# Performance work log

Measured on AMD Instinct MI355X. Metric: run time of the kernel, lower is better.

## Reference

```python
import jax, jax.numpy as jnp
import numpy as np

D = 128   # hidden_size
L = 50    # mailbox length (USER_MAX_LEN / ITEM_MAX_LEN)
NU = 8192 # num user nodes
NI = 8192 # num item nodes


def setup_inputs() -> dict:
    key = jax.random.key(0)
    ks = jax.random.split(key, 16)
    s = 0.05
    return {
        "user": jax.random.normal(ks[0], (NU, D), jnp.float32),
        "item": jax.random.normal(ks[1], (NI, D), jnp.float32),
        "W_user": jax.random.normal(ks[2], (D, D), jnp.float32) * s,
        "W_item": jax.random.normal(ks[3], (D, D), jnp.float32) * s,
        "agg_gate_user": jax.random.normal(ks[4], (2 * D, D), jnp.float32) * s,
        "agg_gate_item": jax.random.normal(ks[5], (2 * D, D), jnp.float32) * s,
        "update_user": jax.random.normal(ks[6], (2 * D, D), jnp.float32) * s,
        "update_item": jax.random.normal(ks[7], (2 * D, D), jnp.float32) * s,
        "user_date_emb": jax.random.normal(ks[8], (L, D), jnp.float32) * s,
        "user_date_emb_k": jax.random.normal(ks[9], (L, D), jnp.float32) * s,
        "item_date_emb": jax.random.normal(ks[10], (L, D), jnp.float32) * s,
        "item_date_emb_k": jax.random.normal(ks[11], (L, D), jnp.float32) * s,
        "user_nbr": jax.random.randint(ks[12], (NU, L), 0, NI, jnp.int64) if jax.config.jax_enable_x64 else jax.random.randint(ks[12], (NU, L), 0, NI, jnp.int32),
        "user_nbr_time": jax.random.randint(ks[13], (NU, L), 0, 1000000, jnp.int32),
        "item_nbr": jax.random.randint(ks[14], (NI, L), 0, NU, jnp.int32),
        "item_nbr_time": jax.random.randint(ks[15], (NI, L), 0, 1000000, jnp.int32),
    }


def _reduce(dst_h, src_mail, time, emb, emb_k, gate_W):
    # dst_h: [N,d], src_mail: [N,L,d], time: [N,L]
    # double argsort -> rank; reorder = L - rank - 1 (time-order position)
    order = jnp.argsort(jnp.argsort(time, axis=1), axis=1)
    reorder = time.shape[1] - order - 1                     # [N,L]
    scale = 1.0 / jnp.sqrt(jnp.asarray(dst_h.shape[-1], dst_h.dtype))
    # long-term attention with positional injection
    e = jnp.sum((emb[reorder] + src_mail) * dst_h[:, None, :], axis=-1) * scale
    alpha = jax.nn.softmax(e, axis=1)                       # [N,L]
    h_long = jnp.einsum('nl,nld->nd', alpha, src_mail + emb_k[reorder])
    # short-term attention against most-recent neighbor
    last = jnp.argmax(time, axis=1)                         # [N]
    last_emb = jnp.take_along_axis(src_mail, last[:, None, None], axis=1)  # [N,1,d]
    e1 = jnp.sum(last_emb * src_mail, axis=-1) * scale
    alpha1 = jax.nn.softmax(e1, axis=1)
    h_short = jnp.einsum('nl,nld->nd', alpha1, src_mail)
    return jnp.concatenate([h_long, h_short], axis=-1) @ gate_W  # [N,d]


def reference(user, item, W_user, W_item, agg_gate_user, agg_gate_item,
              update_user, update_item, user_date_emb, user_date_emb_k,
              item_date_emb, item_date_emb_k, user_nbr, user_nbr_time,
              item_nbr, item_nbr_time):
    # feat_drop/attn_drop are identity (eval mode)
    uh = user @ W_user   # [NU,d]
    ih = item @ W_item   # [NI,d]
    # user nodes aggregate item-neighbor mailboxes
    user_agg = _reduce(uh, ih[user_nbr], user_nbr_time,
                       user_date_emb, user_date_emb_k, agg_gate_user)
    # item nodes aggregate user-neighbor mailboxes
    item_agg = _reduce(ih, uh[item_nbr], item_nbr_time,
                       item_date_emb, item_date_emb_k, agg_gate_item)
    user_out = jnp.tanh(jnp.concatenate([user_agg, user], axis=-1) @ update_user)
    item_out = jnp.tanh(jnp.concatenate([item_agg, item], axis=-1) @ update_item)
    return user_out, item_out
```

## Files before the change

### kernel.cpp

```cpp
#include <hip/hip_runtime.h>
#include <math.h>

#define D 128
#define L 50
#define SCALE 0.08838834764831845f

using bf16x8 = __attribute__((ext_vector_type(8))) short;
using f32x4  = __attribute__((ext_vector_type(4))) float;

__device__ __forceinline__ unsigned f2bf(float x) {
    union { float f; unsigned u; } v; v.f = x;
    return (v.u + 0x7fffu + ((v.u >> 16) & 1u)) >> 16;
}
__device__ __forceinline__ float bflo(unsigned u) {
    union { unsigned u; float f; } v; v.u = u << 16; return v.f;
}
__device__ __forceinline__ float bfhi(unsigned u) {
    union { unsigned u; float f; } v; v.u = u & 0xffff0000u; return v.f;
}

__global__ __launch_bounds__(256) void prep1_kernel(
    const float* __restrict__ Wu, const float* __restrict__ Wi,
    const float* __restrict__ ue, const float* __restrict__ ie,
    const float* __restrict__ gu, const float* __restrict__ gi,
    const float* __restrict__ uu, const float* __restrict__ ui,
    float* __restrict__ GUu, float* __restrict__ GUi,
    unsigned short* __restrict__ Bptu, unsigned short* __restrict__ Bpti,
    unsigned short* __restrict__ Btu, unsigned short* __restrict__ Bti)
{
    int b = blockIdx.x, t = threadIdx.x;
    if (b < 50) {
        int side = b / 25;
        int o = (b % 25) * 256 + t;
        int d = o / L, l = o % L;
        const float* W = side ? Wi : Wu;
        const float* E = side ? ie : ue;
        unsigned short* Bpt = side ? Bpti : Bptu;
        float a = 0.f;
        for (int k = 0; k < D; ++k) a += W[d * D + k] * E[l * D + k];
        Bpt[(128 + l) * 128 + d] = (unsigned short)f2bf(a);
    } else if (b < 306) {
        int bb = b - 50;
        int side = bb / 128;
        int o = (bb % 128) * 256 + t;
        int r = o >> 7, c = o & 127;
        const float* G = side ? gi : gu;
        const float* U = side ? ui : uu;
        float* GU      = side ? GUi : GUu;
        unsigned short* Bt = side ? Bti : Btu;
        float a = 0.f;
        for (int k = 0; k < D; ++k) a += G[r * D + k] * U[k * D + c];
        GU[r * D + c] = a;
        Bt[c * 448 + r] = (unsigned short)f2bf(a);
    } else if (b < 434) {
        int bb = b - 306;
        int side = bb >> 6;
        int o = (bb & 63) * 256 + t;
        int r = o >> 7, c = o & 127;
        const float* U = side ? ui : uu;
        unsigned short* Bt = side ? Bti : Btu;
        Bt[c * 448 + 320 + r] = (unsigned short)f2bf(U[(128 + r) * D + c]);
        if (r < 14) Bt[c * 448 + 306 + r] = 0;
    } else if (b < 562) {
        int bb = b - 434;
        int side = bb >> 6;
        int o = (bb & 63) * 256 + t;
        int k = o >> 7, c = o & 127;
        const float* W = side ? Wi : Wu;
        unsigned short* Bpt = side ? Bpti : Bptu;
        Bpt[c * 128 + k] = (unsigned short)f2bf(W[k * D + c]);
    } else {
        int side = b - 562;
        unsigned short* Bpt = side ? Bpti : Bptu;
        for (int j = 0; j < 7; ++j)
            Bpt[178 * 128 + t * 7 + j] = 0;
    }
}

__global__ __launch_bounds__(256) void prep2_kernel(
    const float* __restrict__ uek, const float* __restrict__ iek,
    const float* __restrict__ GUu, const float* __restrict__ GUi,
    unsigned short* __restrict__ Btu, unsigned short* __restrict__ Bti)
{
    int b = blockIdx.x, t = threadIdx.x;
    int side = b / 25;
    int o = (b % 25) * 256 + t;
    int r = o >> 7, c = o & 127;
    const float* EK = side ? iek : uek;
    const float* GU = side ? GUi : GUu;
    unsigned short* Bt = side ? Bti : Btu;
    float a = 0.f;
    for (int k = 0; k < D; ++k) a += EK[r * D + k] * GU[k * D + c];
    Bt[c * 448 + 256 + r] = (unsigned short)f2bf(a);
}

__global__ __launch_bounds__(256) void proj_mfma(
    const float* __restrict__ Xu, const float* __restrict__ Xi,
    const unsigned* __restrict__ Bptu32, const unsigned* __restrict__ Bpti32,
    unsigned* __restrict__ h32, float* __restrict__ eproj,
    unsigned* __restrict__ A32, int NU)
{
    __shared__ __align__(16) unsigned As[32 * 20];
    __shared__ __align__(16) unsigned Bs[192 * 20];
    int t = threadIdx.x;
    int nb = blockIdx.x * 32;
    const float* X = (nb < NU) ? Xu : Xi;
    int xoff = (nb < NU) ? 0 : NU;
    const unsigned* Bt = (nb < NU) ? Bptu32 : Bpti32;
    int wave = t >> 6, lane = t & 63;
    int m16 = lane & 15, quad = lane >> 4;

    f32x4 acc[2][3];
    for (int i = 0; i < 2; ++i)
        for (int j = 0; j < 3; ++j) acc[i][j] = (f32x4){0.f, 0.f, 0.f, 0.f};

    for (int kc = 0; kc < 4; ++kc) {
        if (t < 128) {
            int row = t >> 2, q = t & 3;
            int n = nb + row;
            const float* src = &X[(size_t)(n - xoff) * D + kc * 32 + q * 8];
            float4 v0 = *(const float4*)&src[0];
            float4 v1 = *(const float4*)&src[4];
            uint4 pk;
            pk.x = f2bf(v0.x) | (f2bf(v0.y) << 16);
            pk.y = f2bf(v0.z) | (f2bf(v0.w) << 16);
            pk.z = f2bf(v1.x) | (f2bf(v1.y) << 16);
            pk.w = f2bf(v1.z) | (f2bf(v1.w) << 16);
            *(uint4*)&As[row * 20 + q * 4] = pk;
            *(uint4*)&A32[(size_t)n * 224 + 160 + kc * 16 + q * 4] = pk;
        }
        #pragma unroll
        for (int i = 0; i < 3; ++i) {
            int idx = t * 3 + i;
            int c = idx >> 2, q = idx & 3;
            uint4 v = *(const uint4*)&Bt[(size_t)c * 64 + kc * 16 + q * 4];
            *(uint4*)&Bs[c * 20 + q * 4] = v;
        }
        __syncthreads();
        bf16x8 a0 = *(const bf16x8*)&As[m16 * 20 + quad * 4];
        bf16x8 a1 = *(const bf16x8*)&As[(16 + m16) * 20 + quad * 4];
        #pragma unroll
        for (int ni = 0; ni < 3; ++ni) {
            bf16x8 bb = *(const bf16x8*)&Bs[(wave * 48 + ni * 16 + m16) * 20 + quad * 4];
            acc[0][ni] = __builtin_amdgcn_mfma_f32_16x16x32_bf16(a0, bb, acc[0][ni], 0, 0, 0);
            acc[1][ni] = __builtin_amdgcn_mfma_f32_16x16x32_bf16(a1, bb, acc[1][ni], 0, 0, 0);
        }
        __syncthreads();
    }
    #pragma unroll
    for (int mi = 0; mi < 2; ++mi)
        #pragma unroll
        for (int ni = 0; ni < 3; ++ni) {
            int col = wave * 48 + ni * 16 + m16;
            #pragma unroll
            for (int r = 0; r < 4; ++r) {
                float me = acc[mi][ni][r];
                float pr = __shfl_xor(me, 1);
                int row = nb + mi * 16 + quad * 4 + r;
                if (col < 128) {
                    if (!(lane & 1))
                        h32[(size_t)row * 64 + (col >> 1)] = f2bf(me) | (f2bf(pr) << 16);
                } else if (col < 178) {
                    eproj[(size_t)row * L + (col - 128)] = me;
                }
            }
        }
}

__global__ __launch_bounds__(256) void agg_kernel(
    const unsigned* __restrict__ h32, const float* __restrict__ eproj,
    const int* __restrict__ unbr, const int* __restrict__ untime,
    const int* __restrict__ inbr, const int* __restrict__ intime,
    unsigned* __restrict__ A32, int NU, int NI)
{
    __shared__ unsigned smail[2][L * 64];
    __shared__ unsigned shb[2][64];
    __shared__ float salpha[2][L], salpha1[2][L];
    __shared__ int stime[2][L], sreorder[2][L], snbr[2][L], slast[2];

    int tb = threadIdx.x;
    int sub = tb >> 7;
    int t = tb & 127;
    int g = blockIdx.x * 2 + sub;
    int wave = t >> 6, lane = t & 63;

    const unsigned* mail; const int* nbrp; const int* timp;
    if (g < NU) { mail = h32 + (size_t)NU * 64; nbrp = unbr + (size_t)g * L;        timp = untime + (size_t)g * L; }
    else        { mail = h32;                   nbrp = inbr + (size_t)(g - NU) * L; timp = intime + (size_t)(g - NU) * L; }

    if (t < 64) shb[sub][t] = h32[(size_t)g * 64 + t];
    if (t < L) { stime[sub][t] = timp[t]; snbr[sub][t] = nbrp[t]; }
    __syncthreads();

    if (t < L) {
        int ti = stime[sub][t]; int rank = 0; bool firstmax = true;
        for (int j = 0; j < L; ++j) {
            int tj = stime[sub][j];
            rank += (tj < ti) || (tj == ti && j < t);
            firstmax = firstmax && ((tj < ti) || (tj == ti && j >= t));
        }
        sreorder[sub][t] = L - 1 - rank;
        if (firstmax) slast[sub] = t;
    }
    {
        int q = t >> 5, p = t & 31;
        #pragma unroll
        for (int i = 0; i < 13; ++i) {
            int l = i * 4 + q;
            if (l < L) {
                uint2 v = *(const uint2*)&mail[(size_t)snbr[sub][l] * 64 + p * 2];
                *(uint2*)&smail[sub][l * 64 + 2 * (p ^ (l & 31))] = v;
            }
        }
    }
    __syncthreads();

    float sc = -1e30f;
    if (lane < L) {
        int xr = lane & 31;
        const unsigned* mrow = &smail[sub][lane * 64];
        if (wave == 0) {
            float a = 0.f;
            for (int p = 0; p < 32; ++p) {
                uint2 mv = *(const uint2*)&mrow[2 * (p ^ xr)];
                uint2 sv = *(const uint2*)&shb[sub][2 * p];
                a += bflo(mv.x) * bflo(sv.x) + bfhi(mv.x) * bfhi(sv.x)
                   + bflo(mv.y) * bflo(sv.y) + bfhi(mv.y) * bfhi(sv.y);
            }
            sc = (a + eproj[(size_t)g * L + sreorder[sub][lane]]) * SCALE;
        } else {
            int li = slast[sub], xl = li & 31;
            const unsigned* lrow = &smail[sub][li * 64];
            float a1 = 0.f;
            for (int p = 0; p < 32; ++p) {
                uint2 mv = *(const uint2*)&mrow[2 * (p ^ xr)];
                uint2 lv = *(const uint2*)&lrow[2 * (p ^ xl)];
                a1 += bflo(mv.x) * bflo(lv.x) + bfhi(mv.x) * bfhi(lv.x)
                    + bflo(mv.y) * bflo(lv.y) + bfhi(mv.y) * bfhi(lv.y);
            }
            sc = a1 * SCALE;
        }
    }
    float mx = sc;
    for (int off = 32; off; off >>= 1) mx = fmaxf(mx, __shfl_xor(mx, off));
    float ex = (lane < L) ? expf(sc - mx) : 0.f;
    float sm = ex;
    for (int off = 32; off; off >>= 1) sm += __shfl_xor(sm, off);
    float al = ex / sm;
    if (lane < L) { if (wave == 0) salpha[sub][lane] = al; else salpha1[sub][lane] = al; }
    __syncthreads();

    {
        const float* alp = wave ? salpha1[sub] : salpha[sub];
        int pr = lane >> 1, bit = lane & 1;
        float ax = 0.f, ay = 0.f;
        for (int l = 0; l < L; ++l) {
            unsigned u = smail[sub][l * 64 + 2 * (pr ^ (l & 31)) + bit];
            float a = alp[l];
            ax += a * bflo(u);
            ay += a * bfhi(u);
        }
        A32[(size_t)g * 224 + wave * 64 + lane] = f2bf(ax) | (f2bf(ay) << 16);
    }
    if (t >= 64 && t < 96) A32[(size_t)g * 224 + 128 + (t - 64)] = 0u;
    __syncthreads();
    if (t < L) {
        ((unsigned short*)A32)[(size_t)g * 448 + 256 + sreorder[sub][t]] =
            (unsigned short)f2bf(salpha[sub][t]);
    }
}

__global__ __launch_bounds__(256) void gemm_out_mfma(
    const unsigned* __restrict__ A32,
    const unsigned* __restrict__ Btu32, const unsigned* __restrict__ Bti32,
    float* __restrict__ out, int NU)
{
    __shared__ __align__(16) unsigned As[32 * 20];
    __shared__ __align__(16) unsigned Bs[128 * 20];
    int t = threadIdx.x;
    int nb = blockIdx.x * 32;
    const unsigned* Bt = (nb < NU) ? Btu32 : Bti32;
    int wave = t >> 6, lane = t & 63;
    int m16 = lane & 15, quad = lane >> 4;
    int ncol0 = wave * 32;

    f32x4 acc[2][2] = {{{0.f, 0.f, 0.f, 0.f}, {0.f, 0.f, 0.f, 0.f}},
                       {{0.f, 0.f, 0.f, 0.f}, {0.f, 0.f, 0.f, 0.f}}};

    for (int kc = 0; kc < 14; ++kc) {
        if (t < 128) {
            int row = t >> 2, q = t & 3;
            uint4 v = *(const uint4*)&A32[(size_t)(nb + row) * 224 + kc * 16 + q * 4];
            *(uint4*)&As[row * 20 + q * 4] = v;
        }
        #pragma unroll
        for (int i = 0; i < 2; ++i) {
            int idx = t * 2 + i;
            int n = idx >> 2, q = idx & 3;
            uint4 v = *(const uint4*)&Bt[(size_t)n * 224 + kc * 16 + q * 4];
            *(uint4*)&Bs[n * 20 + q * 4] = v;
        }
        __syncthreads();
        bf16x8 a0 = *(const bf16x8*)&As[m16 * 20 + quad * 4];
        bf16x8 a1 = *(const bf16x8*)&As[(16 + m16) * 20 + quad * 4];
        bf16x8 b0 = *(const bf16x8*)&Bs[(ncol0 + m16) * 20 + quad * 4];
        bf16x8 b1 = *(const bf16x8*)&Bs[(ncol0 + 16 + m16) * 20 + quad * 4];
        acc[0][0] = __builtin_amdgcn_mfma_f32_16x16x32_bf16(a0, b0, acc[0][0], 0, 0, 0);
        acc[0][1] = __builtin_amdgcn_mfma_f32_16x16x32_bf16(a0, b1, acc[0][1], 0, 0, 0);
        acc[1][0] = __builtin_amdgcn_mfma_f32_16x16x32_bf16(a1, b0, acc[1][0], 0, 0, 0);
        acc[1][1] = __builtin_amdgcn_mfma_f32_16x16x32_bf16(a1, b1, acc[1][1], 0, 0, 0);
        __syncthreads();
    }
    #pragma unroll
    for (int mi = 0; mi < 2; ++mi)
        #pragma unroll
        for (int ni = 0; ni < 2; ++ni)
            #pragma unroll
            for (int r = 0; r < 4; ++r) {
                int row = nb + mi * 16 + quad * 4 + r;
                int col = ncol0 + ni * 16 + m16;
                out[(size_t)row * D + col] = tanhf(acc[mi][ni][r]);
            }
}

extern "C" void kernel_launch(void* const* d_in, const int* in_sizes, int n_in,
                              void* d_out, int out_size, void* d_ws, size_t ws_size,
                              hipStream_t stream) {
    const float* user   = (const float*)d_in[0];
    const float* item   = (const float*)d_in[1];
    const float* Wu     = (const float*)d_in[2];
    const float* Wi     = (const float*)d_in[3];
    const float* gate_u = (const float*)d_in[4];
    const float* gate_i = (const float*)d_in[5];
    const float* upd_u  = (const float*)d_in[6];
    const float* upd_i  = (const float*)d_in[7];
    const float* uemb   = (const float*)d_in[8];
    const float* uembk  = (const float*)d_in[9];
    const float* iemb   = (const float*)d_in[10];
    const float* iembk  = (const float*)d_in[11];
    const int*   unbr   = (const int*)d_in[12];
    const int*   untime = (const int*)d_in[13];
    const int*   inbr   = (const int*)d_in[14];
    const int*   intime = (const int*)d_in[15];

    int NU = in_sizes[0] / D;
    int NI = in_sizes[1] / D;
    int N  = NU + NI;

    float* eproj  = (float*)d_ws;
    float* GUu    = eproj + (size_t)N * L;
    float* GUi    = GUu + 256 * D;
    unsigned* h32   = (unsigned*)(GUi + 256 * D);
    unsigned* A32   = h32 + (size_t)N * 64;
    unsigned* Btu32 = A32 + (size_t)N * 224;
    unsigned* Bti32 = Btu32 + 128 * 224;
    unsigned* Bptu32 = Bti32 + 128 * 224;
    unsigned* Bpti32 = Bptu32 + 192 * 64;

    prep1_kernel<<<564, 256, 0, stream>>>(Wu, Wi, uemb, iemb, gate_u, gate_i,
                                          upd_u, upd_i, GUu, GUi,
                                          (unsigned short*)Bptu32,
                                          (unsigned short*)Bpti32,
                                          (unsigned short*)Btu32,
                                          (unsigned short*)Bti32);
    prep2_kernel<<<50, 256, 0, stream>>>(uembk, iembk, GUu, GUi,
                                         (unsigned short*)Btu32,
                                         (unsigned short*)Bti32);
    proj_mfma<<<N / 32, 256, 0, stream>>>(user, item, Bptu32, Bpti32,
                                          h32, eproj, A32, NU);
    agg_kernel<<<N / 2, 256, 0, stream>>>(h32, eproj, unbr, untime, inbr,
                                          intime, A32, NU, NI);
    gemm_out_mfma<<<N / 32, 256, 0, stream>>>(A32, Btu32, Bti32,
                                              (float*)d_out, NU);
}
```

Measured before the change: 192.7 us.

## Compute attention scores with MFMA and fold prep kernels into one launch

The agg kernel's per-lane scalar bf16 dot products for long- and short-term scores are replaced by MFMA 16x16x32 bf16 ops. The B operand supplies the destination vector in one column and the most recent mailbox row in another. The shared mailbox layout switches from an XOR swizzle to a padded row stride of 66 words to avoid bank conflicts. The second prep kernel is merged into the first by recomputing emb_k·gate·update through a shared-memory intermediate, which removes one launch and the GU workspace. The MFMA path wastes most of the output columns and clamps rows beyond 49, and it adds an extra barrier per block.

Result: faster. 173.7 us (-9.9%).

```diff
diff --git a/kernel.cpp b/kernel.cpp
--- a/kernel.cpp
+++ b/kernel.cpp
@@ -8,6 +8,8 @@
 using bf16x8 = __attribute__((ext_vector_type(8))) short;
 using f32x4  = __attribute__((ext_vector_type(4))) float;
 
+union FragU { bf16x8 f; uint2 u2[2]; };
+
 __device__ __forceinline__ unsigned f2bf(float x) {
     union { float f; unsigned u; } v; v.f = x;
     return (v.u + 0x7fffu + ((v.u >> 16) & 1u)) >> 16;
@@ -19,15 +21,16 @@
     union { unsigned u; float f; } v; v.u = u & 0xffff0000u; return v.f;
 }
 
-__global__ __launch_bounds__(256) void prep1_kernel(
+__global__ __launch_bounds__(256) void prep_all_kernel(
     const float* __restrict__ Wu, const float* __restrict__ Wi,
     const float* __restrict__ ue, const float* __restrict__ ie,
     const float* __restrict__ gu, const float* __restrict__ gi,
     const float* __restrict__ uu, const float* __restrict__ ui,
-    float* __restrict__ GUu, float* __restrict__ GUi,
+    const float* __restrict__ uek, const float* __restrict__ iek,
     unsigned short* __restrict__ Bptu, unsigned short* __restrict__ Bpti,
     unsigned short* __restrict__ Btu, unsigned short* __restrict__ Bti)
 {
+    __shared__ float T[2][128];
     int b = blockIdx.x, t = threadIdx.x;
     if (b < 50) {
         int side = b / 25;
@@ -46,11 +49,9 @@
         int r = o >> 7, c = o & 127;
         const float* G = side ? gi : gu;
         const float* U = side ? ui : uu;
-        float* GU      = side ? GUi : GUu;
         unsigned short* Bt = side ? Bti : Btu;
         float a = 0.f;
         for (int k = 0; k < D; ++k) a += G[r * D + k] * U[k * D + c];
-        GU[r * D + c] = a;
         Bt[c * 448 + r] = (unsigned short)f2bf(a);
     } else if (b < 434) {
         int bb = b - 306;
@@ -69,29 +70,28 @@
         const float* W = side ? Wi : Wu;
         unsigned short* Bpt = side ? Bpti : Bptu;
         Bpt[c * 128 + k] = (unsigned short)f2bf(W[k * D + c]);
-    } else {
+    } else if (b < 564) {
         int side = b - 562;
         unsigned short* Bpt = side ? Bpti : Bptu;
         for (int j = 0; j < 7; ++j)
             Bpt[178 * 128 + t * 7 + j] = 0;
-    }
-}
-
-__global__ __launch_bounds__(256) void prep2_kernel(
-    const float* __restrict__ uek, const float* __restrict__ iek,
-    const float* __restrict__ GUu, const float* __restrict__ GUi,
-    unsigned short* __restrict__ Btu, unsigned short* __restrict__ Bti)
-{
-    int b = blockIdx.x, t = threadIdx.x;
-    int side = b / 25;
-    int o = (b % 25) * 256 + t;
-    int r = o >> 7, c = o & 127;
-    const float* EK = side ? iek : uek;
-    const float* GU = side ? GUi : GUu;
-    unsigned short* Bt = side ? Bti : Btu;
-    float a = 0.f;
-    for (int k = 0; k < D; ++k) a += EK[r * D + k] * GU[k * D + c];
-    Bt[c * 448 + 256 + r] = (unsigned short)f2bf(a);
+    } else {
+        int bb = b - 564;
+        int side = bb / 25;
+        int ro = (bb % 25) * 2;
+        const float* EK = side ? iek : uek;
+        const float* G  = side ? gi : gu;
+        const float* U  = side ? ui : uu;
+        unsigned short* Bt = side ? Bti : Btu;
+        int r = t >> 7, c = t & 127;
+        float a = 0.f;
+        for (int k = 0; k < D; ++k) a += EK[(ro + r) * D + k] * G[k * D + c];
+        T[r][c] = a;
+        __syncthreads();
+        float e = 0.f;
+        for (int j = 0; j < D; ++j) e += T[r][j] * U[j * D + c];
+        Bt[c * 448 + 256 + ro + r] = (unsigned short)f2bf(e);
+    }
 }
 
 __global__ __launch_bounds__(256) void proj_mfma(
@@ -173,8 +173,9 @@
     const int* __restrict__ inbr, const int* __restrict__ intime,
     unsigned* __restrict__ A32, int NU, int NI)
 {
-    __shared__ unsigned smail[2][L * 64];
+    __shared__ unsigned smail[2][L * 66];
     __shared__ unsigned shb[2][64];
+    __shared__ float se2[2][2][64];
     __shared__ float salpha[2][L], salpha1[2][L];
     __shared__ int stime[2][L], sreorder[2][L], snbr[2][L], slast[2];
 
@@ -183,6 +184,7 @@
     int t = tb & 127;
     int g = blockIdx.x * 2 + sub;
     int wave = t >> 6, lane = t & 63;
+    int m16 = lane & 15, quad = lane >> 4;
 
     const unsigned* mail; const int* nbrp; const int* timp;
     if (g < NU) { mail = h32 + (size_t)NU * 64; nbrp = unbr + (size_t)g * L;        timp = untime + (size_t)g * L; }
@@ -209,7 +211,38 @@
             int l = i * 4 + q;
             if (l < L) {
                 uint2 v = *(const uint2*)&mail[(size_t)snbr[sub][l] * 64 + p * 2];
-                *(uint2*)&smail[sub][l * 64 + 2 * (p ^ (l & 31))] = v;
+                *(uint2*)&smail[sub][l * 66 + 2 * p] = v;
+            }
+        }
+    }
+    __syncthreads();
+
+    {
+        const unsigned* bptr = (m16 == 1) ? &smail[sub][slast[sub] * 66]
+                                          : &shb[sub][0];
+        int s0 = wave * 32 + m16;  if (s0 > 49) s0 = 49;
+        int s1 = wave * 32 + 16 + m16;  if (s1 > 49) s1 = 49;
+        const unsigned* a0p = &smail[sub][s0 * 66];
+        const unsigned* a1p = &smail[sub][s1 * 66];
+        f32x4 d0 = {0.f, 0.f, 0.f, 0.f}, d1 = {0.f, 0.f, 0.f, 0.f};
+        #pragma unroll
+        for (int kc = 0; kc < 4; ++kc) {
+            int off = kc * 16 + quad * 4;
+            FragU bf_, af0, af1;
+            bf_.u2[0] = *(const uint2*)&bptr[off];
+            bf_.u2[1] = *(const uint2*)&bptr[off + 2];
+            af0.u2[0] = *(const uint2*)&a0p[off];
+            af0.u2[1] = *(const uint2*)&a0p[off + 2];
+            af1.u2[0] = *(const uint2*)&a1p[off];
+            af1.u2[1] = *(const uint2*)&a1p[off + 2];
+            d0 = __builtin_amdgcn_mfma_f32_16x16x32_bf16(af0.f, bf_.f, d0, 0, 0, 0);
+            d1 = __builtin_amdgcn_mfma_f32_16x16x32_bf16(af1.f, bf_.f, d1, 0, 0, 0);
+        }
+        if (m16 < 2) {
+            #pragma unroll
+            for (int r = 0; r < 4; ++r) {
+                se2[sub][m16][wave * 32 + quad * 4 + r]      = d0[r];
+                se2[sub][m16][wave * 32 + 16 + quad * 4 + r] = d1[r];
             }
         }
     }
@@ -217,29 +250,9 @@
 
     float sc = -1e30f;
     if (lane < L) {
-        int xr = lane & 31;
-        const unsigned* mrow = &smail[sub][lane * 64];
-        if (wave == 0) {
-            float a = 0.f;
-            for (int p = 0; p < 32; ++p) {
-                uint2 mv = *(const uint2*)&mrow[2 * (p ^ xr)];
-                uint2 sv = *(const uint2*)&shb[sub][2 * p];
-                a += bflo(mv.x) * bflo(sv.x) + bfhi(mv.x) * bfhi(sv.x)
-                   + bflo(mv.y) * bflo(sv.y) + bfhi(mv.y) * bfhi(sv.y);
-            }
-            sc = (a + eproj[(size_t)g * L + sreorder[sub][lane]]) * SCALE;
-        } else {
-            int li = slast[sub], xl = li & 31;
-            const unsigned* lrow = &smail[sub][li * 64];
-            float a1 = 0.f;
-            for (int p = 0; p < 32; ++p) {
-                uint2 mv = *(const uint2*)&mrow[2 * (p ^ xr)];
-                uint2 lv = *(const uint2*)&lrow[2 * (p ^ xl)];
-                a1 += bflo(mv.x) * bflo(lv.x) + bfhi(mv.x) * bfhi(lv.x)
-                    + bflo(mv.y) * bflo(lv.y) + bfhi(mv.y) * bfhi(lv.y);
-            }
-            sc = a1 * SCALE;
-        }
+        sc = (wave == 0)
+           ? (se2[sub][0][lane] + eproj[(size_t)g * L + sreorder[sub][lane]]) * SCALE
+           : se2[sub][1][lane] * SCALE;
     }
     float mx = sc;
     for (int off = 32; off; off >>= 1) mx = fmaxf(mx, __shfl_xor(mx, off));
@@ -252,10 +265,10 @@
 
     {
         const float* alp = wave ? salpha1[sub] : salpha[sub];
-        int pr = lane >> 1, bit = lane & 1;
+        const unsigned* base = &smail[sub][lane];
         float ax = 0.f, ay = 0.f;
         for (int l = 0; l < L; ++l) {
-            unsigned u = smail[sub][l * 64 + 2 * (pr ^ (l & 31)) + bit];
+            unsigned u = base[l * 66];
             float a = alp[l];
             ax += a * bflo(u);
             ay += a * bfhi(u);
@@ -348,24 +361,19 @@
     int N  = NU + NI;
 
     float* eproj  = (float*)d_ws;
-    float* GUu    = eproj + (size_t)N * L;
-    float* GUi    = GUu + 256 * D;
-    unsigned* h32   = (unsigned*)(GUi + 256 * D);
+    unsigned* h32   = (unsigned*)(eproj + (size_t)N * L);
     unsigned* A32   = h32 + (size_t)N * 64;
     unsigned* Btu32 = A32 + (size_t)N * 224;
     unsigned* Bti32 = Btu32 + 128 * 224;
     unsigned* Bptu32 = Bti32 + 128 * 224;
     unsigned* Bpti32 = Bptu32 + 192 * 64;
 
-    prep1_kernel<<<564, 256, 0, stream>>>(Wu, Wi, uemb, iemb, gate_u, gate_i,
-                                          upd_u, upd_i, GUu, GUi,
-                                          (unsigned short*)Bptu32,
-                                          (unsigned short*)Bpti32,
-                                          (unsigned short*)Btu32,
-                                          (unsigned short*)Bti32);
-    prep2_kernel<<<50, 256, 0, stream>>>(uembk, iembk, GUu, GUi,
-                                         (unsigned short*)Btu32,
-                                         (unsigned short*)Bti32);
+    prep_all_kernel<<<614, 256, 0, stream>>>(Wu, Wi, uemb, iemb, gate_u, gate_i,
+                                             upd_u, upd_i, uembk, iembk,
+                                             (unsigned short*)Bptu32,
+                                             (unsigned short*)Bpti32,
+                                             (unsigned short*)Btu32,
+                                             (unsigned short*)Bti32);
     proj_mfma<<<N / 32, 256, 0, stream>>>(user, item, Bptu32, Bpti32,
                                           h32, eproj, A32, NU);
     agg_kernel<<<N / 2, 256, 0, stream>>>(h32, eproj, unbr, untime, inbr,
```
